# Performance work log

Measured on AMD Instinct MI355X. Metric: run time of the kernel, lower is better.

## Reference

```python
import jax, jax.numpy as jnp
import numpy as np
from jax import lax

SCALES = [2 ** i for i in range(9)]  # h_grid_global(9, 2**8): dyadic scales 1..256
EPS = 2e-5


def conv1d(x, w, dil, pad):
    # x: [B, Cin, X], w: [Cout, Cin, k]; 'same'-style padding pad on each side, rhs dilation dil
    return lax.conv_general_dilated(x, w, window_strides=(1,), padding=[(pad, pad)],
                                    rhs_dilation=(dil,), dimension_numbers=('NCH', 'OIH', 'NCH'))


def maxpool2_x(x):
    # max pool kernel=2 stride=2 over last (spatial) axis, floor mode like torch
    L = x.shape[-1]
    L2 = (L // 2) * 2
    x = x[..., :L2]
    return jnp.max(x.reshape(x.shape[:-1] + (L2 // 2, 2)), axis=-1)


def lift_conv(x, w):
    k = w.shape[-1]
    outs = [conv1d(x, w, s, s * (k // 2)) / s for s in SCALES]
    return jnp.stack(outs, axis=2)


def gg_conv(x, w):
    # GConvGG with h_crop: x [B, Cin, H, X], w [Cout, Cin, nh=3, k] -> [B, Cout, H-2, X]
    # output scale index i uses input scale slabs i..i+2, x-dilation = scale_i, 1/scale_i normalization
    B, Cin, H, X = x.shape
    Cout, _, nh, k = w.shape
    wf = w.reshape(Cout, Cin * nh, k)
    outs = []
    for i in range(H - nh + 1):
        xi = x[:, :, i:i + nh, :].reshape(B, Cin * nh, X)
        s = SCALES[i]
        outs.append(conv1d(xi, wf, s, s * (k // 2)) / s)
    return jnp.stack(outs, axis=2)


def batchnorm(x, g, b):
    # BatchNorm2d (training batch stats, biased var) over [B, C, H, X]
    m = jnp.mean(x, axis=(0, 2, 3), keepdims=True)
    v = jnp.mean((x - m) ** 2, axis=(0, 2, 3), keepdims=True)
    gb = g[None, :, None, None]
    bb = b[None, :, None, None]
    return gb * (x - m) * lax.rsqrt(v + EPS) + bb


def _winit(key, shape):
    fan = int(np.prod(shape[1:]))
    return jax.random.normal(key, shape, dtype=jnp.float32) * (fan ** -0.5)


def setup_inputs() -> dict:
    key = jax.random.key(0)
    ks = jax.random.split(key, 12)
    B = 4096
    nc = 12
    x = jax.random.normal(ks[0], (B, 100, 6), dtype=jnp.float32)
    inp = {
        'x': x,
        'w1': _winit(ks[1], (nc, 6, 7)),
        'w2': _winit(ks[2], (nc * 2, nc, 3, 5)),
        'w3': _winit(ks[3], (nc * 4, nc * 2, 3, 5)),
        'w4': _winit(ks[4], (nc * 8, nc * 4, 3, 3)),
        'g1': jnp.ones((nc,), jnp.float32), 'b1': jnp.zeros((nc,), jnp.float32),
        'g2': jnp.ones((nc * 2,), jnp.float32), 'b2': jnp.zeros((nc * 2,), jnp.float32),
        'g3': jnp.ones((nc * 4,), jnp.float32), 'b3': jnp.zeros((nc * 4,), jnp.float32),
        'g4': jnp.ones((nc * 8,), jnp.float32), 'b4': jnp.zeros((nc * 8,), jnp.float32),
        'f1w': _winit(ks[5], (nc * 8, nc * 8 * 3)), 'f1b': jnp.zeros((nc * 8,), jnp.float32),
        'f2w': _winit(ks[6], (nc * 4, nc * 8)), 'f2b': jnp.zeros((nc * 4,), jnp.float32),
        'f3w': _winit(ks[7], (6, nc * 4)), 'f3b': jnp.zeros((6,), jnp.float32),
    }
    return inp


def reference(x, w1, w2, w3, w4, g1, b1, g2, b2, g3, b3, g4, b4,
              f1w, f1b, f2w, f2b, f3w, f3b):
    h = jnp.transpose(x, (0, 2, 1))          # [B, 6, 100]
    h = lift_conv(h, w1)                     # [B, 12, 9, 100]
    h = maxpool2_x(h)                        # [B, 12, 9, 50]
    h = batchnorm(jax.nn.relu(h), g1, b1)
    h = maxpool2_x(h)                        # [B, 12, 9, 25]
    h = gg_conv(h, w2)                       # [B, 24, 7, 25]
    h = maxpool2_x(h)                        # [B, 24, 7, 12]
    h = batchnorm(jax.nn.relu(h), g2, b2)
    h = maxpool2_x(h)                        # [B, 24, 7, 6]
    h = gg_conv(h, w3)                       # [B, 48, 5, 6]
    h = maxpool2_x(h)                        # [B, 48, 5, 3]
    h = batchnorm(jax.nn.relu(h), g3, b3)
    h = gg_conv(h, w4)                       # [B, 96, 3, 3]
    h = maxpool2_x(h)                        # [B, 96, 3, 1]
    h = batchnorm(jax.nn.relu(h), g4, b4)
    h = h.reshape(h.shape[0], -1)            # [B, 288]
    h = h @ f1w.T + f1b                      # dropout is identity in eval
    h = h @ f2w.T + f2b
    return h @ f3w.T + f3b                   # [B, 6]
```

## Files before the change

### kernel.cpp

```cpp
#include <hip/hip_runtime.h>
#include <hip/hip_fp16.h>

#define EPSBN 2e-5f

typedef _Float16 hf2 __attribute__((ext_vector_type(2)));

static __device__ __forceinline__ float fdot2h(hf2 a, hf2 b, float c) {
  return __builtin_amdgcn_fdot2(a, b, c, false);
}
static __device__ __forceinline__ unsigned pk(float a, float b) {
  union { __half2 h; unsigned u; } u;
  u.h = __floats2half2_rn(a, b);
  return u.u;
}
static __device__ __forceinline__ float2 uph(unsigned v) {
  union { unsigned u; __half2 h; } x; x.u = v;
  return __half22float2(x.h);
}

#define NB1 4
template<int SI>
__device__ __forceinline__ void s1_si(const unsigned* __restrict__ xsu, int bb, int t0,
    const unsigned* __restrict__ wlu, int o0, bool act, int b,
    __half* __restrict__ r1, float& ts0, float& tq0, float& ts1, float& tq1) {
  constexpr int S = 1 << SI;
  float a0[10], a1[10];
#pragma unroll
  for (int k = 0; k < 10; ++k) { a0[k] = 0.f; a1[k] = 0.f; }
#pragma unroll 1
  for (int cp = 0; cp < 3; ++cp) {
    const hf2* xr = (const hf2*)xsu + (bb * 3 + cp) * 295 + 96 + t0;
    const unsigned* wp = wlu + cp * 84;
#pragma unroll
    for (int j = 0; j < 7; ++j) {
      const int off = S * (j - 3);
      if (off < -96 || off > 98) continue;
      hf2 w0 = *(const hf2*)(wp + j * 12 + o0);
      hf2 w1 = *(const hf2*)(wp + j * 12 + o0 + 1);
      hf2 xv[10];
#pragma unroll
      for (int k = 0; k < 10; ++k) xv[k] = xr[off + k];
#pragma unroll
      for (int k = 0; k < 10; ++k) {
        a0[k] = fdot2h(xv[k], w0, a0[k]);
        a1[k] = fdot2h(xv[k], w1, a1[k]);
      }
    }
  }
  if (act) {
    const float inv = 1.0f / (float)S;
    size_t rb = ((size_t)b * 12 + o0) * 9 + SI;
#pragma unroll
    for (int u = 0; u < 5; ++u) {
      float v0 = fmaxf(fmaxf(a0[2 * u], a0[2 * u + 1]) * inv, 0.f);
      float v1 = fmaxf(fmaxf(a1[2 * u], a1[2 * u + 1]) * inv, 0.f);
      r1[rb * 50 + (t0 >> 1) + u] = __float2half_rn(v0);
      r1[(rb + 9) * 50 + (t0 >> 1) + u] = __float2half_rn(v1);
      ts0 += v0; tq0 += v0 * v0; ts1 += v1; tq1 += v1 * v1;
    }
  }
}

__global__ __launch_bounds__(256) void k_lift(const float* __restrict__ x,
    const float* __restrict__ w1, const float* __restrict__ w2,
    const float* __restrict__ w3, const float* __restrict__ w4,
    __half* __restrict__ W2P, __half* __restrict__ W3P, __half* __restrict__ W4P,
    __half* __restrict__ r1, float* __restrict__ sum, float* __restrict__ sq) {
  __shared__ __align__(16) unsigned xsu[NB1 * 885];
  __shared__ __align__(16) unsigned wlu[252];
  __shared__ float ssum[12], ssq[12];
  int b0 = blockIdx.x * NB1, tid = threadIdx.x;
  {
    int gi = blockIdx.x * 256 + tid;
    if (gi < 4320) {
      int ci = gi & 1, r = gi >> 1, o = r % 24, j = (r / 24) % 5, h = (r / 120) % 3, cp = r / 360;
      int c = 2 * cp + ci;
      W2P[gi] = __float2half_rn(w2[((o * 12 + c) * 3 + h) * 5 + j]);
    } else if (gi < 21600) {
      int k = gi - 4320;
      int ci = k & 1, r = k >> 1, o = r % 48, j = (r / 48) % 5, h = (r / 240) % 3, cp = r / 720;
      int c = 2 * cp + ci;
      W3P[k] = __float2half_rn(w3[((o * 24 + c) * 3 + h) * 5 + j]);
    } else if (gi < 63072) {
      int k = gi - 21600;
      int ci = k & 1, r = k >> 1, o48 = r % 48, j = (r / 48) % 3, h = (r / 144) % 3;
      int cp = (r / 432) % 24, ch = r / 10368, c = 2 * cp + ci, o = ch * 48 + o48;
      W4P[k] = __float2half_rn(w4[((o * 48 + c) * 3 + h) * 3 + j]);
    }
  }
  for (int i = tid; i < NB1 * 885; i += 256) xsu[i] = 0u;
  for (int i = tid; i < 252; i += 256) {
    int cp = i / 84, j = (i % 84) / 12, o = i % 12;
    wlu[i] = pk(w1[(o * 6 + 2 * cp) * 7 + j], w1[(o * 6 + 2 * cp + 1) * 7 + j]);
  }
  if (tid < 12) { ssum[tid] = 0.f; ssq[tid] = 0.f; }
  __syncthreads();
  __half* xsh = (__half*)xsu;
  for (int i = tid; i < NB1 * 600; i += 256) {
    int bb = i / 600, f = i % 600, t = f / 6, c = f % 6;
    xsh[((bb * 3 + (c >> 1)) * 295 + 96 + t) * 2 + (c & 1)] =
        __float2half_rn(x[(size_t)(b0 + bb) * 600 + f]);
  }
  __syncthreads();
  bool act = tid < 240;
  int task = act ? tid : 0;
  int bb = task / 60, r = task % 60;
  int op = r / 10, tc = r % 10;
  int o0 = op * 2, t0 = tc * 10;
  int b = b0 + bb;
  float ts0 = 0.f, tq0 = 0.f, ts1 = 0.f, tq1 = 0.f;
  s1_si<0>(xsu, bb, t0, wlu, o0, act, b, r1, ts0, tq0, ts1, tq1);
  s1_si<1>(xsu, bb, t0, wlu, o0, act, b, r1, ts0, tq0, ts1, tq1);
  s1_si<2>(xsu, bb, t0, wlu, o0, act, b, r1, ts0, tq0, ts1, tq1);
  s1_si<3>(xsu, bb, t0, wlu, o0, act, b, r1, ts0, tq0, ts1, tq1);
  s1_si<4>(xsu, bb, t0, wlu, o0, act, b, r1, ts0, tq0, ts1, tq1);
  s1_si<5>(xsu, bb, t0, wlu, o0, act, b, r1, ts0, tq0, ts1, tq1);
  s1_si<6>(xsu, bb, t0, wlu, o0, act, b, r1, ts0, tq0, ts1, tq1);
  s1_si<7>(xsu, bb, t0, wlu, o0, act, b, r1, ts0, tq0, ts1, tq1);
  s1_si<8>(xsu, bb, t0, wlu, o0, act, b, r1, ts0, tq0, ts1, tq1);
  if (act) {
    atomicAdd(&ssum[o0], ts0); atomicAdd(&ssq[o0], tq0);
    atomicAdd(&ssum[o0 + 1], ts1); atomicAdd(&ssq[o0 + 1], tq1);
  }
  __syncthreads();
  if (tid < 12) { atomicAdd(&sum[tid], ssum[tid]); atomicAdd(&sq[tid], ssq[tid]); }
}

#define NB2 5
template<int S, int I2>
__device__ __forceinline__ void s2_do(const unsigned* __restrict__ abu,
    const unsigned* __restrict__ wlu, int op, bool act, int b,
    unsigned* __restrict__ r2p, float& ts0, float& tq0, float& ts1, float& tq1) {
  float acc0[24], acc1[24];
#pragma unroll
  for (int t = 0; t < 24; ++t) { acc0[t] = 0.f; acc1[t] = 0.f; }
#pragma unroll 1
  for (int cp = 0; cp < 6; ++cp) {
#pragma unroll
    for (int h = 0; h < 3; ++h) {
      const hf2* ar = (const hf2*)(abu + (cp * 9 + I2 + h) * 26);
      hf2 rr[25];
#pragma unroll
      for (int t = 0; t < 25; ++t) rr[t] = ar[t];
      const unsigned* wp = wlu + ((cp * 3 + h) * 5) * 24 + op * 2;
#pragma unroll
      for (int j = 0; j < 5; ++j) {
        const int off = S * (j - 2);
        if (off <= -25 || off >= 25) continue;
        hf2 w0 = *(const hf2*)(wp + j * 24);
        hf2 w1 = *(const hf2*)(wp + j * 24 + 1);
#pragma unroll
        for (int t = 0; t < 24; ++t) {
          if (t + off >= 0 && t + off < 25) {
            acc0[t] = fdot2h(rr[t + off], w0, acc0[t]);
            acc1[t] = fdot2h(rr[t + off], w1, acc1[t]);
          }
        }
      }
    }
  }
  if (act) {
    const float inv = 1.0f / (float)S;
    unsigned* pd = r2p + ((size_t)b * 12 + op) * 42 + I2 * 6;
    float m0 = 0.f, m1 = 0.f;
#pragma unroll
    for (int u = 0; u < 12; ++u) {
      float v0 = fmaxf(fmaxf(acc0[2 * u], acc0[2 * u + 1]) * inv, 0.f);
      float v1 = fmaxf(fmaxf(acc1[2 * u], acc1[2 * u + 1]) * inv, 0.f);
      ts0 += v0; tq0 += v0 * v0; ts1 += v1; tq1 += v1 * v1;
      if ((u & 1) == 0) { m0 = v0; m1 = v1; }
      else pd[u >> 1] = pk(fmaxf(m0, v0), fmaxf(m1, v1));
    }
  }
}

__global__ __launch_bounds__(256) void k_stage2(const __half* __restrict__ r1,
    const __half* __restrict__ W2P,
    const float* __restrict__ SUM, const float* __restrict__ SQ,
    const float* __restrict__ g, const float* __restrict__ bbn, float invN,
    unsigned* __restrict__ r2p, float* __restrict__ sum, float* __restrict__ sq, int B) {
  __shared__ __align__(16) unsigned asu[NB2 * 1405];
  __shared__ __align__(16) unsigned wlu[2160];
  __shared__ float ssum[24], ssq[24];
  __shared__ float scf[12], shf[12];
  int b0 = blockIdx.x * NB2, tid = threadIdx.x;
  if (tid < 12) {
    float m = SUM[tid] * invN;
    float v = SQ[tid] * invN - m * m;
    float scale = g[tid] * rsqrtf(v + EPSBN);
    scf[tid] = scale; shf[tid] = bbn[tid] - m * scale;
    ssum[tid] = 0.f; ssq[tid] = 0.f;
    ssum[tid + 12] = 0.f; ssq[tid + 12] = 0.f;
  }
  __syncthreads();
  for (int i = tid; i < NB2 * 1350; i += 256) {
    int bb = i / 1350, s = i % 1350;
    if (b0 + bb < B) {
      int cp = s / 225, rem = s % 225, row = rem / 25, t = rem % 25;
      int c0 = 2 * cp, c1 = c0 + 1;
      float2 a0 = __half22float2(*(const __half2*)(r1 +
          (((size_t)(b0 + bb) * 12 + c0) * 9 + row) * 50 + 2 * t));
      float2 a1 = __half22float2(*(const __half2*)(r1 +
          (((size_t)(b0 + bb) * 12 + c1) * 9 + row) * 50 + 2 * t));
      float v0 = fmaxf(a0.x, a0.y) * scf[c0] + shf[c0];
      float v1 = fmaxf(a1.x, a1.y) * scf[c1] + shf[c1];
      asu[bb * 1405 + (cp * 9 + row) * 26 + t] = pk(v0, v1);
    }
  }
  for (int i = tid; i < 540; i += 256)
    ((uint4*)wlu)[i] = ((const uint4*)W2P)[i];
  __syncthreads();
  int wv = tid >> 6, lane = tid & 63;
  int bb = lane / 12, op = lane % 12;
  bool act = (lane < 60) && (b0 + bb < B);
  if (bb > 4) bb = 4;
  const unsigned* abu = asu + bb * 1405;
  int b = b0 + bb;
  float ts0 = 0.f, tq0 = 0.f, ts1 = 0.f, tq1 = 0.f;
  if (wv == 0) {
    s2_do<1, 0>(abu, wlu, op, act, b, r2p, ts0, tq0, ts1, tq1);
  } else if (wv == 1) {
    s2_do<2, 1>(abu, wlu, op, act, b, r2p, ts0, tq0, ts1, tq1);
    s2_do<64, 6>(abu, wlu, op, act, b, r2p, ts0, tq0, ts1, tq1);
  } else if (wv == 2) {
    s2_do<4, 2>(abu, wlu, op, act, b, r2p, ts0, tq0, ts1, tq1);
    s2_do<32, 5>(abu, wlu, op, act, b, r2p, ts0, tq0, ts1, tq1);
  } else {
    s2_do<8, 3>(abu, wlu, op, act, b, r2p, ts0, tq0, ts1, tq1);
    s2_do<16, 4>(abu, wlu, op, act, b, r2p, ts0, tq0, ts1, tq1);
  }
  if (act) {
    int o0 = op * 2;
    atomicAdd(&ssum[o0], ts0); atomicAdd(&ssq[o0], tq0);
    atomicAdd(&ssum[o0 + 1], ts1); atomicAdd(&ssq[o0 + 1], tq1);
  }
  __syncthreads();
  if (tid < 24) { atomicAdd(&sum[tid], ssum[tid]); atomicAdd(&sq[tid], ssq[tid]); }
}

#define NB3 8
template<int I2>
__device__ __forceinline__ void s3h(const hf2* __restrict__ rr, int h,
    const hf2* __restrict__ w0, const hf2* __restrict__ w1, float* __restrict__ acc) {
  constexpr int S = 1 << I2;
  const int base = (I2 + h) * 6;
#pragma unroll
  for (int j = 0; j < 5; ++j) {
    const int off = S * (j - 2);
    if (off <= -6 || off >= 6) continue;
#pragma unroll
    for (int t = 0; t < 6; ++t) {
      if (t + off >= 0 && t + off < 6) {
        acc[t] = fdot2h(rr[base + t + off], w0[j], acc[t]);
        acc[6 + t] = fdot2h(rr[base + t + off], w1[j], acc[6 + t]);
      }
    }
  }
}

__global__ __launch_bounds__(256) void k_stage3(const unsigned* __restrict__ r2p,
    const __half* __restrict__ W3P,
    const float* __restrict__ SUM, const float* __restrict__ SQ,
    const float* __restrict__ g, const float* __restrict__ bbn, float invN,
    unsigned* __restrict__ r3, float* __restrict__ sum, float* __restrict__ sq) {
  __shared__ __align__(16) unsigned asu[NB3 * 505];
  __shared__ __align__(16) unsigned wlu[8640];
  __shared__ float ssum[48], ssq[48];
  __shared__ float scf[24], shf[24];
  int b0 = blockIdx.x * NB3, tid = threadIdx.x;
  if (tid < 24) {
    float m = SUM[tid] * invN;
    float v = SQ[tid] * invN - m * m;
    float scale = g[tid] * rsqrtf(v + EPSBN);
    scf[tid] = scale; shf[tid] = bbn[tid] - m * scale;
  }
  if (tid < 48) { ssum[tid] = 0.f; ssq[tid] = 0.f; }
  __syncthreads();
  for (int i = tid; i < NB3 * 504; i += 256) {
    int bb = i / 504, f = i % 504, cp = f / 42;
    int c0 = 2 * cp, c1 = c0 + 1;
    float2 a = uph(r2p[(size_t)(b0 + bb) * 504 + f]);
    asu[bb * 505 + f] = pk(a.x * scf[c0] + shf[c0], a.y * scf[c1] + shf[c1]);
  }
  for (int i = tid; i < 2160; i += 256)
    ((uint4*)wlu)[i] = ((const uint4*)W3P)[i];
  __syncthreads();
  bool act = tid < 192;
  int bb = act ? tid / 24 : 0, op = tid % 24;
  int b = b0 + bb;
  if (act) {
    float acc[60];
#pragma unroll
    for (int k = 0; k < 60; ++k) acc[k] = 0.f;
#pragma unroll 1
    for (int cp = 0; cp < 12; ++cp) {
      const hf2* ar = (const hf2*)(asu + bb * 505 + cp * 42);
      hf2 rr[42];
#pragma unroll
      for (int k = 0; k < 42; ++k) rr[k] = ar[k];
#pragma unroll
      for (int h = 0; h < 3; ++h) {
        const unsigned* wp = wlu + (cp * 15 + h * 5) * 48 + op * 2;
        hf2 w0[5], w1[5];
#pragma unroll
        for (int j = 0; j < 5; ++j) {
          w0[j] = *(const hf2*)(wp + j * 48);
          w1[j] = *(const hf2*)(wp + j * 48 + 1);
        }
        s3h<0>(rr, h, w0, w1, acc);
        s3h<1>(rr, h, w0, w1, acc + 12);
        s3h<2>(rr, h, w0, w1, acc + 24);
        s3h<3>(rr, h, w0, w1, acc + 36);
        s3h<4>(rr, h, w0, w1, acc + 48);
      }
    }
    float ts0 = 0.f, tq0 = 0.f, ts1 = 0.f, tq1 = 0.f;
    int ob = op * 2;
#pragma unroll
    for (int i2 = 0; i2 < 5; ++i2) {
      const float inv = 1.0f / (float)(1 << i2);
      size_t rb = ((size_t)b * 24 + op) * 15 + i2 * 3;
#pragma unroll
      for (int u = 0; u < 3; ++u) {
        float v0 = fmaxf(fmaxf(acc[i2 * 12 + 2 * u], acc[i2 * 12 + 2 * u + 1]) * inv, 0.f);
        float v1 = fmaxf(fmaxf(acc[i2 * 12 + 6 + 2 * u], acc[i2 * 12 + 7 + 2 * u]) * inv, 0.f);
        r3[rb + u] = pk(v0, v1);
        ts0 += v0; tq0 += v0 * v0; ts1 += v1; tq1 += v1 * v1;
      }
    }
    atomicAdd(&ssum[ob], ts0); atomicAdd(&ssq[ob], tq0);
    atomicAdd(&ssum[ob + 1], ts1); atomicAdd(&ssq[ob + 1], tq1);
  }
  __syncthreads();
  if (tid < 48) { atomicAdd(&sum[tid], ssum[tid]); atomicAdd(&sq[tid], ssq[tid]); }
}

#define NB4 8
template<int I2>
__device__ __forceinline__ void s4h(const hf2* __restrict__ rr, int h,
    const hf2* __restrict__ w0, const hf2* __restrict__ w1, float* __restrict__ acc) {
  constexpr int S = 1 << I2;
  const int base = (I2 + h) * 3;
#pragma unroll
  for (int j = 0; j < 3; ++j) {
    const int off = S * (j - 1);
    if (off <= -3 || off >= 3) continue;
    if (off >= 0) {
      acc[0] = fdot2h(rr[base + off], w0[j], acc[0]);
      acc[2] = fdot2h(rr[base + off], w1[j], acc[2]);
    }
    const int i1 = 1 + off;
    if (i1 >= 0 && i1 < 3) {
      acc[1] = fdot2h(rr[base + i1], w0[j], acc[1]);
      acc[3] = fdot2h(rr[base + i1], w1[j], acc[3]);
    }
  }
}

__global__ __launch_bounds__(256) void k_stage4(const unsigned* __restrict__ r3,
    const __half* __restrict__ W4P,
    const float* __restrict__ SUM, const float* __restrict__ SQ,
    const float* __restrict__ g, const float* __restrict__ bbn, float invN,
    float* __restrict__ r4, float* __restrict__ sum, float* __restrict__ sq) {
  __shared__ __align__(16) unsigned asu[NB4 * 361];
  __shared__ __align__(16) unsigned wlu[10368];
  __shared__ float ssum[96], ssq[96];
  __shared__ float scf[48], shf[48];
  int b0 = blockIdx.x * NB4, tid = threadIdx.x;
  if (tid < 48) {
    float m = SUM[tid] * invN;
    float v = SQ[tid] * invN - m * m;
    float scale = g[tid] * rsqrtf(v + EPSBN);
    scf[tid] = scale; shf[tid] = bbn[tid] - m * scale;
  }
  if (tid < 96) { ssum[tid] = 0.f; ssq[tid] = 0.f; }
  __syncthreads();
  for (int i = tid; i < NB4 * 360; i += 256) {
    int bb = i / 360, f = i % 360, cp = f / 15;
    int c0 = 2 * cp, c1 = c0 + 1;
    float2 a = uph(r3[(size_t)(b0 + bb) * 360 + f]);
    asu[bb * 361 + f] = pk(a.x * scf[c0] + shf[c0], a.y * scf[c1] + shf[c1]);
  }
  bool act = tid < 192;
  int bb = act ? tid / 24 : 0, op = tid % 24;
  int b = b0 + bb;
  for (int chunk = 0; chunk < 2; ++chunk) {
    __syncthreads();
    for (int i = tid; i < 2592; i += 256)
      ((uint4*)wlu)[i] = ((const uint4*)W4P)[chunk * 2592 + i];
    __syncthreads();
    if (act) {
      float acc[12];
#pragma unroll
      for (int k = 0; k < 12; ++k) acc[k] = 0.f;
#pragma unroll 1
      for (int cp = 0; cp < 24; ++cp) {
        const hf2* ar = (const hf2*)(asu + bb * 361 + cp * 15);
        hf2 rr[15];
#pragma unroll
        for (int k = 0; k < 15; ++k) rr[k] = ar[k];
#pragma unroll
        for (int h = 0; h < 3; ++h) {
          const unsigned* wp = wlu + ((cp * 3 + h) * 3) * 48 + op * 2;
          hf2 w0[3], w1[3];
#pragma unroll
          for (int j = 0; j < 3; ++j) {
            w0[j] = *(const hf2*)(wp + j * 48);
            w1[j] = *(const hf2*)(wp + j * 48 + 1);
          }
          s4h<0>(rr, h, w0, w1, acc);
          s4h<1>(rr, h, w0, w1, acc + 4);
          s4h<2>(rr, h, w0, w1, acc + 8);
        }
      }
      int o0 = chunk * 48 + op * 2;
#pragma unroll
      for (int oo = 0; oo < 2; ++oo) {
        float ts = 0.f, tq = 0.f;
#pragma unroll
        for (int i2 = 0; i2 < 3; ++i2) {
          const float inv = 1.0f / (float)(1 << i2);
          float v = fmaxf(fmaxf(acc[i2 * 4 + oo * 2], acc[i2 * 4 + oo * 2 + 1]) * inv, 0.f);
          r4[(size_t)b * 288 + (o0 + oo) * 3 + i2] = v;
          ts += v; tq += v * v;
        }
        atomicAdd(&ssum[o0 + oo], ts); atomicAdd(&ssq[o0 + oo], tq);
      }
    }
  }
  __syncthreads();
  if (tid < 96) { atomicAdd(&sum[tid], ssum[tid]); atomicAdd(&sq[tid], ssq[tid]); }
}

__global__ __launch_bounds__(256) void k_fc(const float* __restrict__ r4,
    const float* __restrict__ SUM, const float* __restrict__ SQ,
    const float* __restrict__ g, const float* __restrict__ bbn, float invN,
    const float* __restrict__ f1w, const float* __restrict__ f1b,
    const float* __restrict__ f2w, const float* __restrict__ f2b,
    const float* __restrict__ f3w, const float* __restrict__ f3b,
    float* __restrict__ out) {
  __shared__ float v[4][288];
  __shared__ float h1[4][96];
  __shared__ float h2[4][48];
  __shared__ float scf[96], shf[96];
  int b0 = blockIdx.x * 4, tid = threadIdx.x;
  if (tid < 96) {
    float m = SUM[tid] * invN;
    float vv = SQ[tid] * invN - m * m;
    float scale = g[tid] * rsqrtf(vv + EPSBN);
    scf[tid] = scale; shf[tid] = bbn[tid] - m * scale;
  }
  __syncthreads();
  for (int i = tid; i < 4 * 288; i += 256) {
    int bb = i / 288, f = i % 288, c = f / 3;
    v[bb][f] = r4[(size_t)(b0 + bb) * 288 + f] * scf[c] + shf[c];
  }
  __syncthreads();
  for (int d = tid; d < 384; d += 256) {
    int o = d >> 2, bb = d & 3;
    const float* wr = &f1w[o * 288];
    const float* vv = v[bb];
    float acc = f1b[o];
    for (int f = 0; f < 288; ++f) acc += wr[f] * vv[f];
    h1[bb][o] = acc;
  }
  __syncthreads();
  if (tid < 192) {
    int o = tid >> 2, bb = tid & 3;
    const float* wr = &f2w[o * 96];
    float acc = f2b[o];
    for (int f = 0; f < 96; ++f) acc += wr[f] * h1[bb][f];
    h2[bb][o] = acc;
  }
  __syncthreads();
  if (tid < 24) {
    int o = tid >> 2, bb = tid & 3;
    const float* wr = &f3w[o * 48];
    float acc = f3b[o];
    for (int f = 0; f < 48; ++f) acc += wr[f] * h2[bb][f];
    out[(size_t)(b0 + bb) * 6 + o] = acc;
  }
}

extern "C" void kernel_launch(void* const* d_in, const int* in_sizes, int n_in,
                              void* d_out, int out_size, void* d_ws, size_t ws_size,
                              hipStream_t stream) {
  const float* x   = (const float*)d_in[0];
  const float* w1  = (const float*)d_in[1];
  const float* w2  = (const float*)d_in[2];
  const float* w3  = (const float*)d_in[3];
  const float* w4  = (const float*)d_in[4];
  const float* g1  = (const float*)d_in[5];
  const float* b1  = (const float*)d_in[6];
  const float* g2  = (const float*)d_in[7];
  const float* b2  = (const float*)d_in[8];
  const float* g3  = (const float*)d_in[9];
  const float* b3  = (const float*)d_in[10];
  const float* g4  = (const float*)d_in[11];
  const float* b4  = (const float*)d_in[12];
  const float* f1w = (const float*)d_in[13];
  const float* f1b = (const float*)d_in[14];
  const float* f2w = (const float*)d_in[15];
  const float* f2b = (const float*)d_in[16];
  const float* f3w = (const float*)d_in[17];
  const float* f3b = (const float*)d_in[18];
  float* out = (float*)d_out;
  float* ws = (float*)d_ws;

  const int B = 4096;
  float* SUM1 = ws + 0;   float* SQ1 = ws + 12;
  float* SUM2 = ws + 24;  float* SQ2 = ws + 48;
  float* SUM3 = ws + 72;  float* SQ3 = ws + 120;
  float* SUM4 = ws + 168; float* SQ4 = ws + 264;
  __half* H0  = (__half*)(ws + 1024);
  __half* W2P = H0;
  __half* W3P = H0 + 4320;
  __half* W4P = H0 + 21600;
  __half* R1h = H0 + 65536;
  unsigned* R2P = (unsigned*)(R1h + (size_t)B * 5400);
  unsigned* R3D = (unsigned*)R1h;
  float*  R4  = (float*)(R2P + (size_t)B * 504);

  hipMemsetAsync(d_ws, 0, 384 * sizeof(float), stream);

  k_lift<<<B / NB1, 256, 0, stream>>>(x, w1, w2, w3, w4, W2P, W3P, W4P, R1h, SUM1, SQ1);
  k_stage2<<<(B + NB2 - 1) / NB2, 256, 0, stream>>>(R1h, W2P, SUM1, SQ1, g1, b1,
      1.0f / (float)(B * 450), R2P, SUM2, SQ2, B);
  k_stage3<<<B / NB3, 256, 0, stream>>>(R2P, W3P, SUM2, SQ2, g2, b2,
      1.0f / (float)(B * 84), R3D, SUM3, SQ3);
  k_stage4<<<B / NB4, 256, 0, stream>>>(R3D, W4P, SUM3, SQ3, g3, b3,
      1.0f / (float)(B * 15), R4, SUM4, SQ4);
  k_fc<<<B / 4, 256, 0, stream>>>(R4, SUM4, SQ4, g4, b4,
      1.0f / (float)(B * 3), f1w, f1b, f2w, f2b, f3w, f3b, out);
}
```

Before: 299.5 us.

## Split conv reductions across thread pairs and enlarge blocks in conv stages

Each of the lift, stage2, stage3 and stage4 kernels now launches more threads per block. In the lift kernel, two thread groups split the nine scales between them. In stages 2-4, adjacent lanes each take half of the input-channel reduction, and their partial sums are combined with a shuffle-xor before the pooled results are written. The aim is more parallel work and fewer idle threads per block, at the cost of extra shuffles, more threads per block, and half the lanes sitting idle in the epilogue. Register pressure and occupancy may also change under the new launch bounds.

Measured after the change: 313.6 us. +4.7%, slower.

```diff
diff --git a/kernel.cpp b/kernel.cpp
--- a/kernel.cpp
+++ b/kernel.cpp
@@ -61,7 +61,7 @@
   }
 }
 
-__global__ __launch_bounds__(256) void k_lift(const float* __restrict__ x,
+__global__ __launch_bounds__(512) void k_lift(const float* __restrict__ x,
     const float* __restrict__ w1, const float* __restrict__ w2,
     const float* __restrict__ w3, const float* __restrict__ w4,
     __half* __restrict__ W2P, __half* __restrict__ W3P, __half* __restrict__ W4P,
@@ -71,7 +71,7 @@
   __shared__ float ssum[12], ssq[12];
   int b0 = blockIdx.x * NB1, tid = threadIdx.x;
   {
-    int gi = blockIdx.x * 256 + tid;
+    int gi = blockIdx.x * 512 + tid;
     if (gi < 4320) {
       int ci = gi & 1, r = gi >> 1, o = r % 24, j = (r / 24) % 5, h = (r / 120) % 3, cp = r / 360;
       int c = 2 * cp + ci;
@@ -88,36 +88,41 @@
       W4P[k] = __float2half_rn(w4[((o * 48 + c) * 3 + h) * 3 + j]);
     }
   }
-  for (int i = tid; i < NB1 * 885; i += 256) xsu[i] = 0u;
-  for (int i = tid; i < 252; i += 256) {
+  for (int i = tid; i < NB1 * 885; i += 512) xsu[i] = 0u;
+  for (int i = tid; i < 252; i += 512) {
     int cp = i / 84, j = (i % 84) / 12, o = i % 12;
     wlu[i] = pk(w1[(o * 6 + 2 * cp) * 7 + j], w1[(o * 6 + 2 * cp + 1) * 7 + j]);
   }
   if (tid < 12) { ssum[tid] = 0.f; ssq[tid] = 0.f; }
   __syncthreads();
   __half* xsh = (__half*)xsu;
-  for (int i = tid; i < NB1 * 600; i += 256) {
+  for (int i = tid; i < NB1 * 600; i += 512) {
     int bb = i / 600, f = i % 600, t = f / 6, c = f % 6;
     xsh[((bb * 3 + (c >> 1)) * 295 + 96 + t) * 2 + (c & 1)] =
         __float2half_rn(x[(size_t)(b0 + bb) * 600 + f]);
   }
   __syncthreads();
-  bool act = tid < 240;
-  int task = act ? tid : 0;
+  int sg = tid >> 8;
+  int t8 = tid & 255;
+  bool act = t8 < 240;
+  int task = act ? t8 : 0;
   int bb = task / 60, r = task % 60;
   int op = r / 10, tc = r % 10;
   int o0 = op * 2, t0 = tc * 10;
   int b = b0 + bb;
   float ts0 = 0.f, tq0 = 0.f, ts1 = 0.f, tq1 = 0.f;
-  s1_si<0>(xsu, bb, t0, wlu, o0, act, b, r1, ts0, tq0, ts1, tq1);
-  s1_si<1>(xsu, bb, t0, wlu, o0, act, b, r1, ts0, tq0, ts1, tq1);
-  s1_si<2>(xsu, bb, t0, wlu, o0, act, b, r1, ts0, tq0, ts1, tq1);
-  s1_si<3>(xsu, bb, t0, wlu, o0, act, b, r1, ts0, tq0, ts1, tq1);
-  s1_si<4>(xsu, bb, t0, wlu, o0, act, b, r1, ts0, tq0, ts1, tq1);
-  s1_si<5>(xsu, bb, t0, wlu, o0, act, b, r1, ts0, tq0, ts1, tq1);
-  s1_si<6>(xsu, bb, t0, wlu, o0, act, b, r1, ts0, tq0, ts1, tq1);
-  s1_si<7>(xsu, bb, t0, wlu, o0, act, b, r1, ts0, tq0, ts1, tq1);
-  s1_si<8>(xsu, bb, t0, wlu, o0, act, b, r1, ts0, tq0, ts1, tq1);
+  if (sg == 0) {
+    s1_si<0>(xsu, bb, t0, wlu, o0, act, b, r1, ts0, tq0, ts1, tq1);
+    s1_si<1>(xsu, bb, t0, wlu, o0, act, b, r1, ts0, tq0, ts1, tq1);
+    s1_si<2>(xsu, bb, t0, wlu, o0, act, b, r1, ts0, tq0, ts1, tq1);
+    s1_si<8>(xsu, bb, t0, wlu, o0, act, b, r1, ts0, tq0, ts1, tq1);
+  } else {
+    s1_si<3>(xsu, bb, t0, wlu, o0, act, b, r1, ts0, tq0, ts1, tq1);
+    s1_si<4>(xsu, bb, t0, wlu, o0, act, b, r1, ts0, tq0, ts1, tq1);
+    s1_si<5>(xsu, bb, t0, wlu, o0, act, b, r1, ts0, tq0, ts1, tq1);
+    s1_si<6>(xsu, bb, t0, wlu, o0, act, b, r1, ts0, tq0, ts1, tq1);
+    s1_si<7>(xsu, bb, t0, wlu, o0, act, b, r1, ts0, tq0, ts1, tq1);
+  }
   if (act) {
     atomicAdd(&ssum[o0], ts0); atomicAdd(&ssq[o0], tq0);
     atomicAdd(&ssum[o0 + 1], ts1); atomicAdd(&ssq[o0 + 1], tq1);
@@ -129,13 +134,13 @@
 #define NB2 5
 template<int S, int I2>
 __device__ __forceinline__ void s2_do(const unsigned* __restrict__ abu,
-    const unsigned* __restrict__ wlu, int op, bool act, int b,
+    const unsigned* __restrict__ wlu, int op, int cp0, int kh, bool act, int b,
     unsigned* __restrict__ r2p, float& ts0, float& tq0, float& ts1, float& tq1) {
   float acc0[24], acc1[24];
 #pragma unroll
   for (int t = 0; t < 24; ++t) { acc0[t] = 0.f; acc1[t] = 0.f; }
 #pragma unroll 1
-  for (int cp = 0; cp < 6; ++cp) {
+  for (int cp = cp0; cp < cp0 + 3; ++cp) {
 #pragma unroll
     for (int h = 0; h < 3; ++h) {
       const hf2* ar = (const hf2*)(abu + (cp * 9 + I2 + h) * 26);
@@ -160,21 +165,28 @@
     }
   }
   if (act) {
-    const float inv = 1.0f / (float)S;
-    unsigned* pd = r2p + ((size_t)b * 12 + op) * 42 + I2 * 6;
-    float m0 = 0.f, m1 = 0.f;
-#pragma unroll
-    for (int u = 0; u < 12; ++u) {
-      float v0 = fmaxf(fmaxf(acc0[2 * u], acc0[2 * u + 1]) * inv, 0.f);
-      float v1 = fmaxf(fmaxf(acc1[2 * u], acc1[2 * u + 1]) * inv, 0.f);
-      ts0 += v0; tq0 += v0 * v0; ts1 += v1; tq1 += v1 * v1;
-      if ((u & 1) == 0) { m0 = v0; m1 = v1; }
-      else pd[u >> 1] = pk(fmaxf(m0, v0), fmaxf(m1, v1));
-    }
-  }
-}
-
-__global__ __launch_bounds__(256) void k_stage2(const __half* __restrict__ r1,
+#pragma unroll
+    for (int t = 0; t < 24; ++t) {
+      acc0[t] += __shfl_xor(acc0[t], 1);
+      acc1[t] += __shfl_xor(acc1[t], 1);
+    }
+    if (kh == 0) {
+      const float inv = 1.0f / (float)S;
+      unsigned* pd = r2p + ((size_t)b * 12 + op) * 42 + I2 * 6;
+      float m0 = 0.f, m1 = 0.f;
+#pragma unroll
+      for (int u = 0; u < 12; ++u) {
+        float v0 = fmaxf(fmaxf(acc0[2 * u], acc0[2 * u + 1]) * inv, 0.f);
+        float v1 = fmaxf(fmaxf(acc1[2 * u], acc1[2 * u + 1]) * inv, 0.f);
+        ts0 += v0; tq0 += v0 * v0; ts1 += v1; tq1 += v1 * v1;
+        if ((u & 1) == 0) { m0 = v0; m1 = v1; }
+        else pd[u >> 1] = pk(fmaxf(m0, v0), fmaxf(m1, v1));
+      }
+    }
+  }
+}
+
+__global__ __launch_bounds__(512) void k_stage2(const __half* __restrict__ r1,
     const __half* __restrict__ W2P,
     const float* __restrict__ SUM, const float* __restrict__ SQ,
     const float* __restrict__ g, const float* __restrict__ bbn, float invN,
@@ -193,7 +205,7 @@
     ssum[tid + 12] = 0.f; ssq[tid + 12] = 0.f;
   }
   __syncthreads();
-  for (int i = tid; i < NB2 * 1350; i += 256) {
+  for (int i = tid; i < NB2 * 1350; i += 512) {
     int bb = i / 1350, s = i % 1350;
     if (b0 + bb < B) {
       int cp = s / 225, rem = s % 225, row = rem / 25, t = rem % 25;
@@ -207,29 +219,34 @@
       asu[bb * 1405 + (cp * 9 + row) * 26 + t] = pk(v0, v1);
     }
   }
-  for (int i = tid; i < 540; i += 256)
+  for (int i = tid; i < 540; i += 512)
     ((uint4*)wlu)[i] = ((const uint4*)W2P)[i];
   __syncthreads();
   int wv = tid >> 6, lane = tid & 63;
-  int bb = lane / 12, op = lane % 12;
-  bool act = (lane < 60) && (b0 + bb < B);
-  if (bb > 4) bb = 4;
+  int ig = wv >> 1;
+  int kh = lane & 1;
+  int p = ((wv & 1) << 5) + (lane >> 1);
+  bool act = p < 60;
+  int bb = act ? p / 12 : 4;
+  int op = act ? p % 12 : 0;
+  act = act && (b0 + bb < B);
+  int cp0 = kh * 3;
   const unsigned* abu = asu + bb * 1405;
   int b = b0 + bb;
   float ts0 = 0.f, tq0 = 0.f, ts1 = 0.f, tq1 = 0.f;
-  if (wv == 0) {
-    s2_do<1, 0>(abu, wlu, op, act, b, r2p, ts0, tq0, ts1, tq1);
-  } else if (wv == 1) {
-    s2_do<2, 1>(abu, wlu, op, act, b, r2p, ts0, tq0, ts1, tq1);
-    s2_do<64, 6>(abu, wlu, op, act, b, r2p, ts0, tq0, ts1, tq1);
-  } else if (wv == 2) {
-    s2_do<4, 2>(abu, wlu, op, act, b, r2p, ts0, tq0, ts1, tq1);
-    s2_do<32, 5>(abu, wlu, op, act, b, r2p, ts0, tq0, ts1, tq1);
+  if (ig == 0) {
+    s2_do<1, 0>(abu, wlu, op, cp0, kh, act, b, r2p, ts0, tq0, ts1, tq1);
+  } else if (ig == 1) {
+    s2_do<2, 1>(abu, wlu, op, cp0, kh, act, b, r2p, ts0, tq0, ts1, tq1);
+    s2_do<64, 6>(abu, wlu, op, cp0, kh, act, b, r2p, ts0, tq0, ts1, tq1);
+  } else if (ig == 2) {
+    s2_do<4, 2>(abu, wlu, op, cp0, kh, act, b, r2p, ts0, tq0, ts1, tq1);
+    s2_do<32, 5>(abu, wlu, op, cp0, kh, act, b, r2p, ts0, tq0, ts1, tq1);
   } else {
-    s2_do<8, 3>(abu, wlu, op, act, b, r2p, ts0, tq0, ts1, tq1);
-    s2_do<16, 4>(abu, wlu, op, act, b, r2p, ts0, tq0, ts1, tq1);
-  }
-  if (act) {
+    s2_do<8, 3>(abu, wlu, op, cp0, kh, act, b, r2p, ts0, tq0, ts1, tq1);
+    s2_do<16, 4>(abu, wlu, op, cp0, kh, act, b, r2p, ts0, tq0, ts1, tq1);
+  }
+  if (act && kh == 0) {
     int o0 = op * 2;
     atomicAdd(&ssum[o0], ts0); atomicAdd(&ssq[o0], tq0);
     atomicAdd(&ssum[o0 + 1], ts1); atomicAdd(&ssq[o0 + 1], tq1);
@@ -258,7 +275,7 @@
   }
 }
 
-__global__ __launch_bounds__(256) void k_stage3(const unsigned* __restrict__ r2p,
+__global__ __launch_bounds__(384) void k_stage3(const unsigned* __restrict__ r2p,
     const __half* __restrict__ W3P,
     const float* __restrict__ SUM, const float* __restrict__ SQ,
     const float* __restrict__ g, const float* __restrict__ bbn, float invN,
@@ -276,44 +293,49 @@
   }
   if (tid < 48) { ssum[tid] = 0.f; ssq[tid] = 0.f; }
   __syncthreads();
-  for (int i = tid; i < NB3 * 504; i += 256) {
+  for (int i = tid; i < NB3 * 504; i += 384) {
     int bb = i / 504, f = i % 504, cp = f / 42;
     int c0 = 2 * cp, c1 = c0 + 1;
     float2 a = uph(r2p[(size_t)(b0 + bb) * 504 + f]);
     asu[bb * 505 + f] = pk(a.x * scf[c0] + shf[c0], a.y * scf[c1] + shf[c1]);
   }
-  for (int i = tid; i < 2160; i += 256)
+  for (int i = tid; i < 2160; i += 384)
     ((uint4*)wlu)[i] = ((const uint4*)W3P)[i];
   __syncthreads();
-  bool act = tid < 192;
-  int bb = act ? tid / 24 : 0, op = tid % 24;
+  int wv = tid >> 6, lane = tid & 63;
+  int kh = lane & 1;
+  int w = wv * 32 + (lane >> 1);
+  int bb = w / 24, op = w % 24;
   int b = b0 + bb;
-  if (act) {
-    float acc[60];
-#pragma unroll
-    for (int k = 0; k < 60; ++k) acc[k] = 0.f;
+  float acc[60];
+#pragma unroll
+  for (int k = 0; k < 60; ++k) acc[k] = 0.f;
+  int cp0 = kh * 6;
 #pragma unroll 1
-    for (int cp = 0; cp < 12; ++cp) {
-      const hf2* ar = (const hf2*)(asu + bb * 505 + cp * 42);
-      hf2 rr[42];
-#pragma unroll
-      for (int k = 0; k < 42; ++k) rr[k] = ar[k];
-#pragma unroll
-      for (int h = 0; h < 3; ++h) {
-        const unsigned* wp = wlu + (cp * 15 + h * 5) * 48 + op * 2;
-        hf2 w0[5], w1[5];
-#pragma unroll
-        for (int j = 0; j < 5; ++j) {
-          w0[j] = *(const hf2*)(wp + j * 48);
-          w1[j] = *(const hf2*)(wp + j * 48 + 1);
-        }
-        s3h<0>(rr, h, w0, w1, acc);
-        s3h<1>(rr, h, w0, w1, acc + 12);
-        s3h<2>(rr, h, w0, w1, acc + 24);
-        s3h<3>(rr, h, w0, w1, acc + 36);
-        s3h<4>(rr, h, w0, w1, acc + 48);
-      }
-    }
+  for (int cp = cp0; cp < cp0 + 6; ++cp) {
+    const hf2* ar = (const hf2*)(asu + bb * 505 + cp * 42);
+    hf2 rr[42];
+#pragma unroll
+    for (int k = 0; k < 42; ++k) rr[k] = ar[k];
+#pragma unroll
+    for (int h = 0; h < 3; ++h) {
+      const unsigned* wp = wlu + (cp * 15 + h * 5) * 48 + op * 2;
+      hf2 w0[5], w1[5];
+#pragma unroll
+      for (int j = 0; j < 5; ++j) {
+        w0[j] = *(const hf2*)(wp + j * 48);
+        w1[j] = *(const hf2*)(wp + j * 48 + 1);
+      }
+      s3h<0>(rr, h, w0, w1, acc);
+      s3h<1>(rr, h, w0, w1, acc + 12);
+      s3h<2>(rr, h, w0, w1, acc + 24);
+      s3h<3>(rr, h, w0, w1, acc + 36);
+      s3h<4>(rr, h, w0, w1, acc + 48);
+    }
+  }
+#pragma unroll
+  for (int k = 0; k < 60; ++k) acc[k] += __shfl_xor(acc[k], 1);
+  if (kh == 0) {
     float ts0 = 0.f, tq0 = 0.f, ts1 = 0.f, tq1 = 0.f;
     int ob = op * 2;
 #pragma unroll
@@ -357,7 +379,7 @@
   }
 }
 
-__global__ __launch_bounds__(256) void k_stage4(const unsigned* __restrict__ r3,
+__global__ __launch_bounds__(384) void k_stage4(const unsigned* __restrict__ r3,
     const __half* __restrict__ W4P,
     const float* __restrict__ SUM, const float* __restrict__ SQ,
     const float* __restrict__ g, const float* __restrict__ bbn, float invN,
@@ -375,44 +397,49 @@
   }
   if (tid < 96) { ssum[tid] = 0.f; ssq[tid] = 0.f; }
   __syncthreads();
-  for (int i = tid; i < NB4 * 360; i += 256) {
+  for (int i = tid; i < NB4 * 360; i += 384) {
     int bb = i / 360, f = i % 360, cp = f / 15;
     int c0 = 2 * cp, c1 = c0 + 1;
     float2 a = uph(r3[(size_t)(b0 + bb) * 360 + f]);
     asu[bb * 361 + f] = pk(a.x * scf[c0] + shf[c0], a.y * scf[c1] + shf[c1]);
   }
-  bool act = tid < 192;
-  int bb = act ? tid / 24 : 0, op = tid % 24;
+  int wv = tid >> 6, lane = tid & 63;
+  int kh = lane & 1;
+  int w = wv * 32 + (lane >> 1);
+  int bb = w / 24, op = w % 24;
   int b = b0 + bb;
+  int cp0 = kh * 12;
   for (int chunk = 0; chunk < 2; ++chunk) {
     __syncthreads();
-    for (int i = tid; i < 2592; i += 256)
+    for (int i = tid; i < 2592; i += 384)
       ((uint4*)wlu)[i] = ((const uint4*)W4P)[chunk * 2592 + i];
     __syncthreads();
-    if (act) {
-      float acc[12];
-#pragma unroll
-      for (int k = 0; k < 12; ++k) acc[k] = 0.f;
+    float acc[12];
+#pragma unroll
+    for (int k = 0; k < 12; ++k) acc[k] = 0.f;
 #pragma unroll 1
-      for (int cp = 0; cp < 24; ++cp) {
-        const hf2* ar = (const hf2*)(asu + bb * 361 + cp * 15);
-        hf2 rr[15];
-#pragma unroll
-        for (int k = 0; k < 15; ++k) rr[k] = ar[k];
-#pragma unroll
-        for (int h = 0; h < 3; ++h) {
-          const unsigned* wp = wlu + ((cp * 3 + h) * 3) * 48 + op * 2;
-          hf2 w0[3], w1[3];
-#pragma unroll
-          for (int j = 0; j < 3; ++j) {
-            w0[j] = *(const hf2*)(wp + j * 48);
-            w1[j] = *(const hf2*)(wp + j * 48 + 1);
-          }
-          s4h<0>(rr, h, w0, w1, acc);
-          s4h<1>(rr, h, w0, w1, acc + 4);
-          s4h<2>(rr, h, w0, w1, acc + 8);
+    for (int cp = cp0; cp < cp0 + 12; ++cp) {
+      const hf2* ar = (const hf2*)(asu + bb * 361 + cp * 15);
+      hf2 rr[15];
+#pragma unroll
+      for (int k = 0; k < 15; ++k) rr[k] = ar[k];
+#pragma unroll
+      for (int h = 0; h < 3; ++h) {
+        const unsigned* wp = wlu + ((cp * 3 + h) * 3) * 48 + op * 2;
+        hf2 w0[3], w1[3];
+#pragma unroll
+        for (int j = 0; j < 3; ++j) {
+          w0[j] = *(const hf2*)(wp + j * 48);
+          w1[j] = *(const hf2*)(wp + j * 48 + 1);
         }
-      }
+        s4h<0>(rr, h, w0, w1, acc);
+        s4h<1>(rr, h, w0, w1, acc + 4);
+        s4h<2>(rr, h, w0, w1, acc + 8);
+      }
+    }
+#pragma unroll
+    for (int k = 0; k < 12; ++k) acc[k] += __shfl_xor(acc[k], 1);
+    if (kh == 0) {
       int o0 = chunk * 48 + op * 2;
 #pragma unroll
       for (int oo = 0; oo < 2; ++oo) {
@@ -523,12 +550,12 @@
 
   hipMemsetAsync(d_ws, 0, 384 * sizeof(float), stream);
 
-  k_lift<<<B / NB1, 256, 0, stream>>>(x, w1, w2, w3, w4, W2P, W3P, W4P, R1h, SUM1, SQ1);
-  k_stage2<<<(B + NB2 - 1) / NB2, 256, 0, stream>>>(R1h, W2P, SUM1, SQ1, g1, b1,
+  k_lift<<<B / NB1, 512, 0, stream>>>(x, w1, w2, w3, w4, W2P, W3P, W4P, R1h, SUM1, SQ1);
+  k_stage2<<<(B + NB2 - 1) / NB2, 512, 0, stream>>>(R1h, W2P, SUM1, SQ1, g1, b1,
       1.0f / (float)(B * 450), R2P, SUM2, SQ2, B);
-  k_stage3<<<B / NB3, 256, 0, stream>>>(R2P, W3P, SUM2, SQ2, g2, b2,
+  k_stage3<<<B / NB3, 384, 0, stream>>>(R2P, W3P, SUM2, SQ2, g2, b2,
       1.0f / (float)(B * 84), R3D, SUM3, SQ3);
-  k_stage4<<<B / NB4, 256, 0, stream>>>(R3D, W4P, SUM3, SQ3, g3, b3,
+  k_stage4<<<B / NB4, 384, 0, stream>>>(R3D, W4P, SUM3, SQ3, g3, b3,
       1.0f / (float)(B * 15), R4, SUM4, SQ4);
   k_fc<<<B / 4, 256, 0, stream>>>(R4, SUM4, SQ4, g4, b4,
       1.0f / (float)(B * 3), f1w, f1b, f2w, f2b, f3w, f3b, out);
```
